# Optimization experiments

Hardware: AMD Instinct MI355X
Metric: run time of the kernel (lower is better)

Reference implementation:

```python
import jax, jax.numpy as jnp
import numpy as np

MIN_DISP = -112
MAX_DISP = 16


def setup_inputs() -> dict:
    key = jax.random.key(0)
    k1, k2 = jax.random.split(key)
    B, H, W, C = 2, 96, 192, 16
    left = jax.random.normal(k1, (B, H, W, C), dtype=jnp.float32)
    right = jax.random.normal(k2, (B, H, W, C), dtype=jnp.float32)
    return {"left": left, "right": right}


def reference(left, right):
    # Cost-volume construction by disparity-shifted channel concat.
    # For disparity i: out_left[w] = left[w], out_right[w] = right[w - i],
    # both zero-filled where (w - i) is out of [0, W). This reproduces the
    # slice+cat+pad loop of the torch module in one vectorized gather.
    B, H, W, C = left.shape
    disps = jnp.arange(MIN_DISP, MAX_DISP)            # [D]
    w = jnp.arange(W)                                  # [W]
    idx = w[None, :] - disps[:, None]                  # [D, W] source column in right
    valid = (idx >= 0) & (idx < W)                     # [D, W]
    idx_c = jnp.clip(idx, 0, W - 1)
    mask = valid[None, None, :, :, None]               # [1,1,D,W,1]
    right_sh = jnp.where(mask, right[:, :, idx_c, :], 0.0)          # [B,H,D,W,C]
    left_b = jnp.where(mask, left[:, :, None, :, :], 0.0)           # [B,H,D,W,C]
    cv = jnp.concatenate([left_b, right_sh], axis=-1)               # [B,H,D,W,2C]
    return jnp.transpose(cv, (0, 2, 1, 3, 4))                       # [B,D,H,W,2C]
```

## Files before the change

### kernel.cpp

```cpp
#include <hip/hip_runtime.h>


constexpr int B_ = 2;
constexpr int H_ = 96;
constexpr int W_ = 192;
constexpr int D_ = 128;

typedef float v4f __attribute__((ext_vector_type(4)));

__global__ __launch_bounds__(256) void cost_concat_kernel(
    const v4f* __restrict__ left,
    const v4f* __restrict__ right,
    v4f* __restrict__ out)
{
    const int h = blockIdx.x;
    const int d = blockIdx.y;
    const int b = blockIdx.z;

    const int rowBase = (b * H_ + h) * (W_ * 4);
    const long long outBase =
        (((long long)(b * D_ + d)) * H_ + h) * (long long)(W_ * 8);

    const int shift = 112 - d;

    const v4f* __restrict__ lrow = left  + rowBase;
    const v4f* __restrict__ rrow = right + rowBase;
    v4f* __restrict__ orow = out + outBase;

    #pragma unroll
    for (int j = threadIdx.x; j < W_ * 8; j += 256) {
        const int w  = j >> 3;
        const int c4 = j & 7;
        const int idx = w + shift;

        v4f v = (v4f)(0.f);
        if ((unsigned)idx < (unsigned)W_) {
            const v4f* src = (c4 < 4)
                ? (lrow + w   * 4 + c4)
                : (rrow + idx * 4 + (c4 - 4));
            v = *src;
        }
        __builtin_nontemporal_store(v, orow + j);
    }
}

extern "C" void kernel_launch(void* const* d_in, const int* in_sizes, int n_in,
                              void* d_out, int out_size, void* d_ws, size_t ws_size,
                              hipStream_t stream)
{
    const v4f* left  = (const v4f*)d_in[0];
    const v4f* right = (const v4f*)d_in[1];
    v4f* out = (v4f*)d_out;

    dim3 grid(H_, D_, B_);
    cost_concat_kernel<<<grid, 256, 0, stream>>>(left, right, out);
}
```

Baseline: 118.0 us.

## Tile disparities per block and keep left row in registers

Each block now handles 16 consecutive disparities for one (b,h) row instead of one. The left-half values are loaded into registers once and reused across all 16 disparity outputs, and only the shifted right values are re-read. This cuts redundant global reads and block launch overhead, at the cost of fewer blocks and a serial loop over disparities per block.

Measured after the change: 119.7 us. About the same (+1.5%).

```diff
diff --git a/kernel.cpp b/kernel.cpp
--- a/kernel.cpp
+++ b/kernel.cpp
@@ -5,6 +5,8 @@
 constexpr int H_ = 96;
 constexpr int W_ = 192;
 constexpr int D_ = 128;
+constexpr int DT = 16;
+constexpr int NJ = (W_ * 8) / 256;
 
 typedef float v4f __attribute__((ext_vector_type(4)));
 
@@ -13,34 +15,50 @@
     const v4f* __restrict__ right,
     v4f* __restrict__ out)
 {
-    const int h = blockIdx.x;
-    const int d = blockIdx.y;
-    const int b = blockIdx.z;
+    const int h  = blockIdx.x;
+    const int d0 = blockIdx.y * DT;
+    const int b  = blockIdx.z;
+    const int tid = threadIdx.x;
 
     const int rowBase = (b * H_ + h) * (W_ * 4);
-    const long long outBase =
-        (((long long)(b * D_ + d)) * H_ + h) * (long long)(W_ * 8);
-
-    const int shift = 112 - d;
-
     const v4f* __restrict__ lrow = left  + rowBase;
     const v4f* __restrict__ rrow = right + rowBase;
-    v4f* __restrict__ orow = out + outBase;
 
+    const bool isLeft = (tid & 7) < 4;
+    const int  c      = tid & 3;
+
+    int ws[NJ];
+    v4f lv[NJ];
     #pragma unroll
-    for (int j = threadIdx.x; j < W_ * 8; j += 256) {
-        const int w  = j >> 3;
-        const int c4 = j & 7;
-        const int idx = w + shift;
+    for (int k = 0; k < NJ; ++k) {
+        const int j = tid + 256 * k;
+        ws[k] = j >> 3;
+        lv[k] = (v4f)(0.f);
+        if (isLeft) lv[k] = lrow[ws[k] * 4 + c];
+    }
 
-        v4f v = (v4f)(0.f);
-        if ((unsigned)idx < (unsigned)W_) {
-            const v4f* src = (c4 < 4)
-                ? (lrow + w   * 4 + c4)
-                : (rrow + idx * 4 + (c4 - 4));
-            v = *src;
+    long long outBase =
+        (((long long)(b * D_ + d0)) * H_ + h) * (long long)(W_ * 8);
+    const long long dStride = (long long)H_ * (W_ * 8);
+
+    for (int dd = 0; dd < DT; ++dd) {
+        const int shift = 112 - (d0 + dd);
+        v4f* __restrict__ orow = out + outBase;
+
+        #pragma unroll
+        for (int k = 0; k < NJ; ++k) {
+            const int idx = ws[k] + shift;
+            const bool valid = (unsigned)idx < (unsigned)W_;
+
+            v4f v = (v4f)(0.f);
+            if (isLeft) {
+                if (valid) v = lv[k];
+            } else {
+                if (valid) v = rrow[idx * 4 + c];
+            }
+            __builtin_nontemporal_store(v, orow + (tid + 256 * k));
         }
-        __builtin_nontemporal_store(v, orow + j);
+        outBase += dStride;
     }
 }
 
@@ -52,6 +70,6 @@
     const v4f* right = (const v4f*)d_in[1];
     v4f* out = (v4f*)d_out;
 
-    dim3 grid(H_, D_, B_);
+    dim3 grid(H_, D_ / DT, B_);
     cost_concat_kernel<<<grid, 256, 0, stream>>>(left, right, out);
 }
```

## Switch to flat grid-stride kernel with fixed block count

Applied to the files above, without the earlier changes.

Replaces the per-row 3D grid (24576 blocks, 6 iterations each) with a flat grid of 2048 blocks that stride over the whole output with 72 iterations per thread. Each element's indices are recomputed with integer divisions. The aim is to cut block launch and scheduling overhead and keep the store stream going continuously. The cost is extra per-element index arithmetic and fewer blocks available to hide memory latency.

After: 116.9 us, median of 2. About the same (-1.0%).

```diff
diff --git a/kernel.cpp b/kernel.cpp
--- a/kernel.cpp
+++ b/kernel.cpp
@@ -8,39 +8,40 @@
 
 typedef float v4f __attribute__((ext_vector_type(4)));
 
+constexpr unsigned TOTAL4   = 37748736u;
+constexpr unsigned NBLK     = 2048u;
+constexpr unsigned NTHREADS = NBLK * 256u;
+constexpr int      ITERS    = TOTAL4 / NTHREADS;
+
 __global__ __launch_bounds__(256) void cost_concat_kernel(
     const v4f* __restrict__ left,
     const v4f* __restrict__ right,
     v4f* __restrict__ out)
 {
-    const int h = blockIdx.x;
-    const int d = blockIdx.y;
-    const int b = blockIdx.z;
+    unsigned j = blockIdx.x * 256u + threadIdx.x;
 
-    const int rowBase = (b * H_ + h) * (W_ * 4);
-    const long long outBase =
-        (((long long)(b * D_ + d)) * H_ + h) * (long long)(W_ * 8);
+    #pragma unroll 4
+    for (int it = 0; it < ITERS; ++it, j += NTHREADS) {
+        const unsigned rowid = j / 1536u;
+        const unsigned rr    = j - rowid * 1536u;
+        const unsigned w     = rr >> 3;
+        const unsigned c4    = rr & 7u;
+        const unsigned b     = rowid / 12288u;
+        const unsigned t     = rowid - b * 12288u;
+        const unsigned d     = t / 96u;
+        const unsigned h     = t - d * 96u;
 
-    const int shift = 112 - d;
-
-    const v4f* __restrict__ lrow = left  + rowBase;
-    const v4f* __restrict__ rrow = right + rowBase;
-    v4f* __restrict__ orow = out + outBase;
-
-    #pragma unroll
-    for (int j = threadIdx.x; j < W_ * 8; j += 256) {
-        const int w  = j >> 3;
-        const int c4 = j & 7;
-        const int idx = w + shift;
+        const int idx = (int)w + 112 - (int)d;
+        const unsigned rowBase = (b * H_ + h) * (W_ * 4);
 
         v4f v = (v4f)(0.f);
         if ((unsigned)idx < (unsigned)W_) {
-            const v4f* src = (c4 < 4)
-                ? (lrow + w   * 4 + c4)
-                : (rrow + idx * 4 + (c4 - 4));
+            const v4f* src = (c4 < 4u)
+                ? (left  + rowBase + w * 4u + c4)
+                : (right + rowBase + (unsigned)idx * 4u + (c4 - 4u));
             v = *src;
         }
-        __builtin_nontemporal_store(v, orow + j);
+        __builtin_nontemporal_store(v, out + j);
     }
 }
 
@@ -52,6 +53,5 @@
     const v4f* right = (const v4f*)d_in[1];
     v4f* out = (v4f*)d_out;
 
-    dim3 grid(H_, D_, B_);
-    cost_concat_kernel<<<grid, 256, 0, stream>>>(left, right, out);
+    cost_concat_kernel<<<dim3(NBLK), 256, 0, stream>>>(left, right, out);
 }
```
